# Kernel optimization log

Measured on AMD Instinct MI355X. Metric: run time of the kernel, lower is better.

The kernel has to match this reference:

```python
import jax, jax.numpy as jnp
import numpy as np

NUM_GRAPHS = 512

def setup_inputs() -> dict:
    key = jax.random.key(0)
    ks = jax.random.split(key, 16)
    N, E, F_IN, D = 50000, 800000, 128, 64
    x = jax.random.normal(ks[0], (N, F_IN), dtype=jnp.float32)
    edge_index = jax.random.randint(ks[1], (2, E), 0, N, dtype=jnp.int32)
    batch_index = jnp.sort(jax.random.randint(ks[2], (N,), 0, NUM_GRAPHS, dtype=jnp.int32))
    def lin(k, fin, fout):
        s = 1.0 / np.sqrt(fin)
        return jax.random.uniform(k, (fin, fout), jnp.float32, -s, s)
    return {
        "x": x, "edge_index": edge_index, "batch_index": batch_index,
        "W0": lin(ks[3], F_IN, D), "b0": jnp.zeros((D,), jnp.float32),
        "W1": lin(ks[4], D, D), "b1": jnp.zeros((D,), jnp.float32),
        "W2": lin(ks[5], D, D), "b2": jnp.zeros((D,), jnp.float32),
        "W3": lin(ks[6], D, D), "b3": jnp.zeros((D,), jnp.float32),
        "Wout": lin(ks[7], 2 * D, 1), "bout": jnp.zeros((1,), jnp.float32),
    }

def _gcn_edges(edge_index, N):
    # add self-loops and compute symmetric normalization D^-1/2 (A+I) D^-1/2
    loops = jnp.arange(N, dtype=edge_index.dtype)
    row = jnp.concatenate([edge_index[0], loops])  # source
    col = jnp.concatenate([edge_index[1], loops])  # target
    deg = jax.ops.segment_sum(jnp.ones_like(col, dtype=jnp.float32), col, num_segments=N)
    dinv = jnp.where(deg > 0, jax.lax.rsqrt(deg), 0.0)
    norm = dinv[row] * dinv[col]  # [E+N]
    return row, col, norm

def _gcn_conv(h, row, col, norm, W, b, N):
    h = h @ W                                   # [N, D] linear transform first
    msg = h[row] * norm[:, None]                # gather + scale
    out = jax.ops.segment_sum(msg, col, num_segments=N)  # scatter-add
    return out + b

def reference(x, edge_index, batch_index, W0, b0, W1, b1, W2, b2, W3, b3, Wout, bout):
    N = x.shape[0]
    row, col, norm = _gcn_edges(edge_index, N)
    h = jnp.tanh(_gcn_conv(x, row, col, norm, W0, b0, N))
    h = jnp.tanh(_gcn_conv(h, row, col, norm, W1, b1, N))
    h = jnp.tanh(_gcn_conv(h, row, col, norm, W2, b2, N))
    h = jnp.tanh(_gcn_conv(h, row, col, norm, W3, b3, N))
    gmax = jax.ops.segment_max(h, batch_index, num_segments=NUM_GRAPHS)
    gmax = jnp.where(jnp.isfinite(gmax), gmax, 0.0)  # empty segments -> 0
    gsum = jax.ops.segment_sum(h, batch_index, num_segments=NUM_GRAPHS)
    cnt = jax.ops.segment_sum(jnp.ones((N,), jnp.float32), batch_index, num_segments=NUM_GRAPHS)
    gmean = gsum / jnp.maximum(cnt, 1.0)[:, None]
    hidden = jnp.concatenate([gmax, gmean], axis=1)   # [G, 2D]
    out = hidden @ Wout + bout                        # [G, 1]
    return out, hidden
```

## Files before the change

### kernel.cpp

```cpp
#include <hip/hip_runtime.h>
#include <math.h>

#define CAP 64
typedef unsigned short ushort_t;
typedef unsigned int uint_t;

__global__ __launch_bounds__(256) void k_scatter2(const int* __restrict__ row,
                                                  const int* __restrict__ col, int E, int N,
                                                  int* __restrict__ deg, ushort_t* __restrict__ csr) {
    const int part = blockIdx.x & 7;
    const int slot = blockIdx.x >> 3;
    const int nslots = gridDim.x >> 3;
    const int lo = (int)((long long)N * part / 8);
    const int hi = (int)((long long)N * (part + 1) / 8);
    const int nq = E >> 2;
    for (int t = slot * blockDim.x + threadIdx.x; t < nq; t += nslots * blockDim.x) {
        int4 c = ((const int4*)col)[t];
        int4 r = ((const int4*)row)[t];
        if (c.x >= lo && c.x < hi) { int d = atomicAdd(&deg[c.x], 1); if (d < CAP) csr[((size_t)c.x << 6) + d] = (ushort_t)r.x; }
        if (c.y >= lo && c.y < hi) { int d = atomicAdd(&deg[c.y], 1); if (d < CAP) csr[((size_t)c.y << 6) + d] = (ushort_t)r.y; }
        if (c.z >= lo && c.z < hi) { int d = atomicAdd(&deg[c.z], 1); if (d < CAP) csr[((size_t)c.z << 6) + d] = (ushort_t)r.z; }
        if (c.w >= lo && c.w < hi) { int d = atomicAdd(&deg[c.w], 1); if (d < CAP) csr[((size_t)c.w << 6) + d] = (ushort_t)r.w; }
    }
    if (blockIdx.x == 0) {
        for (int e = (nq << 2) + threadIdx.x; e < E; e += blockDim.x) {
            int c = col[e];
            int d = atomicAdd(&deg[c], 1);
            if (d < CAP) csr[((size_t)c << 6) + d] = (ushort_t)row[e];
        }
    }
}

template <int K>
__global__ __launch_bounds__(256) void k_gemm(const float* __restrict__ X,
                                              const float* __restrict__ W,
                                              const int* __restrict__ deg,
                                              float* __restrict__ Gb, int N) {
    __shared__ __align__(16) float Wl[32 * 64];
    __shared__ __align__(16) float Xl[64 * 36];

    const int tid = threadIdx.x;
    const int wave = tid >> 6, lane = tid & 63;
    const int d8 = lane & 7, ns = lane >> 3;
    const int n0 = wave * 16 + ns, n1 = n0 + 8;

    const int base = blockIdx.x * 64;
    if (base >= N) return;
    const int tile_n = min(64, N - base);

    float4 a0l = {0,0,0,0}, a0h = {0,0,0,0}, a1l = {0,0,0,0}, a1h = {0,0,0,0};

    for (int kh = 0; kh < K / 32; kh++) {
        __syncthreads();
        for (int i = tid; i < 512; i += 256)
            ((float4*)Wl)[i] = ((const float4*)(W + kh * 2048))[i];
        for (int idx = tid; idx < 512; idx += 256) {
            int n = idx >> 3, q = idx & 7;
            float4 v = {0,0,0,0};
            if (n < tile_n) v = ((const float4*)(X + (size_t)(base + n) * K + kh * 32))[q];
            ((float4*)(Xl + n * 36))[q] = v;
        }
        __syncthreads();

        const float4* xq0 = (const float4*)(Xl + n0 * 36);
        const float4* xq1 = (const float4*)(Xl + n1 * 36);
        const float* wcol = Wl + d8 * 8;
#pragma unroll
        for (int kq = 0; kq < 8; kq++) {
            const float4 x4a = xq0[kq];
            const float4 x4b = xq1[kq];
            const float xs0[4] = {x4a.x, x4a.y, x4a.z, x4a.w};
            const float xs1[4] = {x4b.x, x4b.y, x4b.z, x4b.w};
#pragma unroll
            for (int j = 0; j < 4; j++) {
                const int k = kq * 4 + j;
                const float4 wa = *(const float4*)(wcol + k * 64);
                const float4 wb = *(const float4*)(wcol + k * 64 + 4);
                const float xa = xs0[j];
                const float xb = xs1[j];
                a0l.x = fmaf(xa, wa.x, a0l.x); a0l.y = fmaf(xa, wa.y, a0l.y);
                a0l.z = fmaf(xa, wa.z, a0l.z); a0l.w = fmaf(xa, wa.w, a0l.w);
                a0h.x = fmaf(xa, wb.x, a0h.x); a0h.y = fmaf(xa, wb.y, a0h.y);
                a0h.z = fmaf(xa, wb.z, a0h.z); a0h.w = fmaf(xa, wb.w, a0h.w);
                a1l.x = fmaf(xb, wa.x, a1l.x); a1l.y = fmaf(xb, wa.y, a1l.y);
                a1l.z = fmaf(xb, wa.z, a1l.z); a1l.w = fmaf(xb, wa.w, a1l.w);
                a1h.x = fmaf(xb, wb.x, a1h.x); a1h.y = fmaf(xb, wb.y, a1h.y);
                a1h.z = fmaf(xb, wb.z, a1h.z); a1h.w = fmaf(xb, wb.w, a1h.w);
            }
        }
    }

    int gn0 = base + n0, gn1 = base + n1;
    if (gn0 < N) {
        float s = rsqrtf((float)(deg[gn0] + 1));
        float4* ptr = (float4*)(Gb + (size_t)gn0 * 64);
        ptr[d8 * 2]     = make_float4(a0l.x * s, a0l.y * s, a0l.z * s, a0l.w * s);
        ptr[d8 * 2 + 1] = make_float4(a0h.x * s, a0h.y * s, a0h.z * s, a0h.w * s);
    }
    if (gn1 < N) {
        float s = rsqrtf((float)(deg[gn1] + 1));
        float4* ptr = (float4*)(Gb + (size_t)gn1 * 64);
        ptr[d8 * 2]     = make_float4(a1l.x * s, a1l.y * s, a1l.z * s, a1l.w * s);
        ptr[d8 * 2 + 1] = make_float4(a1h.x * s, a1h.y * s, a1h.z * s, a1h.w * s);
    }
}

__global__ __launch_bounds__(256) void k_agg(const float* __restrict__ Gb,
                                             const int* __restrict__ deg,
                                             const ushort_t* __restrict__ csr,
                                             const float* __restrict__ bias,
                                             float* __restrict__ H, int N) {
    const int tid = threadIdx.x;
    const int wave = tid >> 6, lane = tid & 63;
    const int s = lane >> 4;
    const int q = lane & 15;
    const int n = blockIdx.x * 16 + wave * 4 + s;
    const bool alive = (n < N);

    int cnt = 0;
    if (alive) { cnt = deg[n]; if (cnt > CAP) cnt = CAP; }
    const ushort_t* rowp = csr + ((size_t)(alive ? n : 0) << 6);

    float4 acc = {0.f, 0.f, 0.f, 0.f};
    if (alive) acc = ((const float4*)(Gb + (size_t)n * 64))[q];

    int i = 0;
    for (; i + 8 <= cnt; i += 8) {
        uint2 qa = *(const uint2*)(rowp + i);
        uint2 qb = *(const uint2*)(rowp + i + 4);
        int j0 = qa.x & 0xffff, j1 = qa.x >> 16, j2 = qa.y & 0xffff, j3 = qa.y >> 16;
        int j4 = qb.x & 0xffff, j5 = qb.x >> 16, j6 = qb.y & 0xffff, j7 = qb.y >> 16;
        float4 g0 = ((const float4*)(Gb + (size_t)j0 * 64))[q];
        float4 g1 = ((const float4*)(Gb + (size_t)j1 * 64))[q];
        float4 g2 = ((const float4*)(Gb + (size_t)j2 * 64))[q];
        float4 g3 = ((const float4*)(Gb + (size_t)j3 * 64))[q];
        float4 g4 = ((const float4*)(Gb + (size_t)j4 * 64))[q];
        float4 g5 = ((const float4*)(Gb + (size_t)j5 * 64))[q];
        float4 g6 = ((const float4*)(Gb + (size_t)j6 * 64))[q];
        float4 g7 = ((const float4*)(Gb + (size_t)j7 * 64))[q];
        float4 t0 = make_float4(g0.x + g1.x, g0.y + g1.y, g0.z + g1.z, g0.w + g1.w);
        float4 t1 = make_float4(g2.x + g3.x, g2.y + g3.y, g2.z + g3.z, g2.w + g3.w);
        float4 t2 = make_float4(g4.x + g5.x, g4.y + g5.y, g4.z + g5.z, g4.w + g5.w);
        float4 t3 = make_float4(g6.x + g7.x, g6.y + g7.y, g6.z + g7.z, g6.w + g7.w);
        acc.x += (t0.x + t1.x) + (t2.x + t3.x);
        acc.y += (t0.y + t1.y) + (t2.y + t3.y);
        acc.z += (t0.z + t1.z) + (t2.z + t3.z);
        acc.w += (t0.w + t1.w) + (t2.w + t3.w);
    }
    if (i + 4 <= cnt) {
        uint2 qa = *(const uint2*)(rowp + i);
        int j0 = qa.x & 0xffff, j1 = qa.x >> 16, j2 = qa.y & 0xffff, j3 = qa.y >> 16;
        float4 g0 = ((const float4*)(Gb + (size_t)j0 * 64))[q];
        float4 g1 = ((const float4*)(Gb + (size_t)j1 * 64))[q];
        float4 g2 = ((const float4*)(Gb + (size_t)j2 * 64))[q];
        float4 g3 = ((const float4*)(Gb + (size_t)j3 * 64))[q];
        acc.x += (g0.x + g1.x) + (g2.x + g3.x);
        acc.y += (g0.y + g1.y) + (g2.y + g3.y);
        acc.z += (g0.z + g1.z) + (g2.z + g3.z);
        acc.w += (g0.w + g1.w) + (g2.w + g3.w);
        i += 4;
    }
    if (i + 2 <= cnt) {
        uint_t qq = *(const uint_t*)(rowp + i);
        int j0 = qq & 0xffff, j1 = qq >> 16;
        float4 g0 = ((const float4*)(Gb + (size_t)j0 * 64))[q];
        float4 g1 = ((const float4*)(Gb + (size_t)j1 * 64))[q];
        acc.x += g0.x + g1.x; acc.y += g0.y + g1.y;
        acc.z += g0.z + g1.z; acc.w += g0.w + g1.w;
        i += 2;
    }
    if (i < cnt) {
        int j0 = rowp[i];
        float4 g0 = ((const float4*)(Gb + (size_t)j0 * 64))[q];
        acc.x += g0.x; acc.y += g0.y; acc.z += g0.z; acc.w += g0.w;
    }

    if (alive) {
        float dinv = rsqrtf((float)(cnt + 1));
        float4 b4 = ((const float4*)bias)[q];
        float4 r;
        r.x = tanhf(fmaf(acc.x, dinv, b4.x));
        r.y = tanhf(fmaf(acc.y, dinv, b4.y));
        r.z = tanhf(fmaf(acc.z, dinv, b4.z));
        r.w = tanhf(fmaf(acc.w, dinv, b4.w));
        ((float4*)(H + (size_t)n * 64))[q] = r;
    }
}

__global__ __launch_bounds__(256) void k_pool(const float* __restrict__ H,
                                              const int* __restrict__ batch, int N, int Gn,
                                              const float* __restrict__ Wout,
                                              const float* __restrict__ bout,
                                              float* __restrict__ out,
                                              float* __restrict__ hidden) {
    int g = blockIdx.x * 4 + (threadIdx.x >> 6);
    if (g >= Gn) return;
    int lane = threadIdx.x & 63;
    int lo = 0, hi = N;
    while (lo < hi) { int m = (lo + hi) >> 1; if (batch[m] < g) lo = m + 1; else hi = m; }
    int s = lo;
    lo = s; hi = N;
    while (lo < hi) { int m = (lo + hi) >> 1; if (batch[m] < g + 1) lo = m + 1; else hi = m; }
    int c = lo - s;

    float m0 = -INFINITY, m1 = -INFINITY, m2 = -INFINITY, m3 = -INFINITY;
    float s0 = 0.f, s1 = 0.f, s2 = 0.f, s3 = 0.f;
    int n = s;
    for (; n + 3 < s + c; n += 4) {
        float v0 = H[(size_t)n * 64 + lane];
        float v1 = H[(size_t)(n + 1) * 64 + lane];
        float v2 = H[(size_t)(n + 2) * 64 + lane];
        float v3 = H[(size_t)(n + 3) * 64 + lane];
        m0 = fmaxf(m0, v0); s0 += v0;
        m1 = fmaxf(m1, v1); s1 += v1;
        m2 = fmaxf(m2, v2); s2 += v2;
        m3 = fmaxf(m3, v3); s3 += v3;
    }
    for (; n < s + c; n++) {
        float v = H[(size_t)n * 64 + lane];
        m0 = fmaxf(m0, v); s0 += v;
    }
    float vmax = fmaxf(fmaxf(m0, m1), fmaxf(m2, m3));
    float vsum = (s0 + s1) + (s2 + s3);
    float gmax = (c > 0) ? vmax : 0.f;
    float gmean = (c > 0) ? vsum / (float)c : 0.f;
    hidden[(size_t)g * 128 + lane] = gmax;
    hidden[(size_t)g * 128 + 64 + lane] = gmean;
    float p = fmaf(gmax, Wout[lane], gmean * Wout[64 + lane]);
    for (int o = 32; o > 0; o >>= 1) p += __shfl_down(p, o);
    if (lane == 0) out[g] = p + bout[0];
}

extern "C" void kernel_launch(void* const* d_in, const int* in_sizes, int n_in,
                              void* d_out, int out_size, void* d_ws, size_t ws_size,
                              hipStream_t stream) {
    const float* x    = (const float*)d_in[0];
    const int*   ei   = (const int*)d_in[1];
    const int*   batch= (const int*)d_in[2];
    const float* W0 = (const float*)d_in[3];  const float* b0 = (const float*)d_in[4];
    const float* W1 = (const float*)d_in[5];  const float* b1 = (const float*)d_in[6];
    const float* W2 = (const float*)d_in[7];  const float* b2 = (const float*)d_in[8];
    const float* W3 = (const float*)d_in[9];  const float* b3 = (const float*)d_in[10];
    const float* Wout = (const float*)d_in[11]; const float* bout = (const float*)d_in[12];

    const int N  = in_sizes[2];
    const int E  = in_sizes[1] / 2;
    const int Gn = out_size / 129;

    const int* row = ei;
    const int* col = ei + E;

    float* out_p    = (float*)d_out;
    float* hidden_p = out_p + Gn;

    char* wp = (char*)d_ws;
    auto alloc = [&](size_t bytes) { void* p = (void*)wp; wp += (bytes + 255) & ~(size_t)255; return p; };
    int*      deg = (int*)alloc((size_t)N * 4);
    ushort_t* csr = (ushort_t*)alloc((size_t)N * CAP * 2);
    float*    Gb  = (float*)alloc((size_t)N * 64 * 4);
    float*    Hb  = (float*)alloc((size_t)N * 64 * 4);

    hipMemsetAsync(deg, 0, (size_t)N * 4, stream);
    k_scatter2<<<2048, 256, 0, stream>>>(row, col, E, N, deg, csr);

    const int gblocks = (N + 63) / 64;
    const int ablocks = (N + 15) / 16;

    k_gemm<128><<<gblocks, 256, 0, stream>>>(x, W0, deg, Gb, N);
    k_agg<<<ablocks, 256, 0, stream>>>(Gb, deg, csr, b0, Hb, N);
    k_gemm<64><<<gblocks, 256, 0, stream>>>(Hb, W1, deg, Gb, N);
    k_agg<<<ablocks, 256, 0, stream>>>(Gb, deg, csr, b1, Hb, N);
    k_gemm<64><<<gblocks, 256, 0, stream>>>(Hb, W2, deg, Gb, N);
    k_agg<<<ablocks, 256, 0, stream>>>(Gb, deg, csr, b2, Hb, N);
    k_gemm<64><<<gblocks, 256, 0, stream>>>(Hb, W3, deg, Gb, N);
    k_agg<<<ablocks, 256, 0, stream>>>(Gb, deg, csr, b3, Hb, N);

    k_pool<<<(Gn + 3) / 4, 256, 0, stream>>>(Hb, batch, N, Gn, Wout, bout, out_p, hidden_p);
}
```

Measured before the change: 327.3 us.

## Retile GEMM to 128 rows per block with 8 row accumulators per thread

The feature-transform GEMM now processes 128 nodes per block instead of 64. Each thread owns 4 output columns for 8 rows, so each weight float4 loaded from LDS is reused across 8 rows, and the output stores are coalesced float4 writes of contiguous columns. The goal is less LDS traffic per FMA and fewer blocks for the same work. In exchange the X tile in shared memory doubles and the kernel needs more accumulator registers.

```diff
diff --git a/kernel.cpp b/kernel.cpp
--- a/kernel.cpp
+++ b/kernel.cpp
@@ -37,71 +37,66 @@
                                               const int* __restrict__ deg,
                                               float* __restrict__ Gb, int N) {
     __shared__ __align__(16) float Wl[32 * 64];
-    __shared__ __align__(16) float Xl[64 * 36];
+    __shared__ __align__(16) float Xl[128 * 36];
 
     const int tid = threadIdx.x;
     const int wave = tid >> 6, lane = tid & 63;
-    const int d8 = lane & 7, ns = lane >> 3;
-    const int n0 = wave * 16 + ns, n1 = n0 + 8;
-
-    const int base = blockIdx.x * 64;
+    const int q = lane & 15;
+    const int s = lane >> 4;
+
+    const int base = blockIdx.x * 128;
     if (base >= N) return;
-    const int tile_n = min(64, N - base);
-
-    float4 a0l = {0,0,0,0}, a0h = {0,0,0,0}, a1l = {0,0,0,0}, a1h = {0,0,0,0};
+    const int tile_n = min(128, N - base);
+
+    float4 acc[8];
+#pragma unroll
+    for (int m = 0; m < 8; m++) acc[m] = make_float4(0.f, 0.f, 0.f, 0.f);
+
+    const int wbase = wave * 32;
 
     for (int kh = 0; kh < K / 32; kh++) {
         __syncthreads();
         for (int i = tid; i < 512; i += 256)
             ((float4*)Wl)[i] = ((const float4*)(W + kh * 2048))[i];
-        for (int idx = tid; idx < 512; idx += 256) {
-            int n = idx >> 3, q = idx & 7;
-            float4 v = {0,0,0,0};
-            if (n < tile_n) v = ((const float4*)(X + (size_t)(base + n) * K + kh * 32))[q];
-            ((float4*)(Xl + n * 36))[q] = v;
+        for (int idx = tid; idx < 1024; idx += 256) {
+            int n = idx >> 3, kq = idx & 7;
+            float4 v = {0.f, 0.f, 0.f, 0.f};
+            if (n < tile_n) v = ((const float4*)(X + (size_t)(base + n) * K + kh * 32))[kq];
+            ((float4*)(Xl + n * 36))[kq] = v;
         }
         __syncthreads();
 
-        const float4* xq0 = (const float4*)(Xl + n0 * 36);
-        const float4* xq1 = (const float4*)(Xl + n1 * 36);
-        const float* wcol = Wl + d8 * 8;
+        const float* wq = Wl + 4 * q;
 #pragma unroll
         for (int kq = 0; kq < 8; kq++) {
-            const float4 x4a = xq0[kq];
-            const float4 x4b = xq1[kq];
-            const float xs0[4] = {x4a.x, x4a.y, x4a.z, x4a.w};
-            const float xs1[4] = {x4b.x, x4b.y, x4b.z, x4b.w};
-#pragma unroll
-            for (int j = 0; j < 4; j++) {
-                const int k = kq * 4 + j;
-                const float4 wa = *(const float4*)(wcol + k * 64);
-                const float4 wb = *(const float4*)(wcol + k * 64 + 4);
-                const float xa = xs0[j];
-                const float xb = xs1[j];
-                a0l.x = fmaf(xa, wa.x, a0l.x); a0l.y = fmaf(xa, wa.y, a0l.y);
-                a0l.z = fmaf(xa, wa.z, a0l.z); a0l.w = fmaf(xa, wa.w, a0l.w);
-                a0h.x = fmaf(xa, wb.x, a0h.x); a0h.y = fmaf(xa, wb.y, a0h.y);
-                a0h.z = fmaf(xa, wb.z, a0h.z); a0h.w = fmaf(xa, wb.w, a0h.w);
-                a1l.x = fmaf(xb, wa.x, a1l.x); a1l.y = fmaf(xb, wa.y, a1l.y);
-                a1l.z = fmaf(xb, wa.z, a1l.z); a1l.w = fmaf(xb, wa.w, a1l.w);
-                a1h.x = fmaf(xb, wb.x, a1h.x); a1h.y = fmaf(xb, wb.y, a1h.y);
-                a1h.z = fmaf(xb, wb.z, a1h.z); a1h.w = fmaf(xb, wb.w, a1h.w);
+            const float4 w0 = *(const float4*)(wq + (kq * 4 + 0) * 64);
+            const float4 w1 = *(const float4*)(wq + (kq * 4 + 1) * 64);
+            const float4 w2 = *(const float4*)(wq + (kq * 4 + 2) * 64);
+            const float4 w3 = *(const float4*)(wq + (kq * 4 + 3) * 64);
+#pragma unroll
+            for (int m = 0; m < 8; m++) {
+                const int ln = wbase + s + 4 * m;
+                const float4 x4 = ((const float4*)(Xl + ln * 36))[kq];
+                acc[m].x = fmaf(x4.x, w0.x, acc[m].x); acc[m].y = fmaf(x4.x, w0.y, acc[m].y);
+                acc[m].z = fmaf(x4.x, w0.z, acc[m].z); acc[m].w = fmaf(x4.x, w0.w, acc[m].w);
+                acc[m].x = fmaf(x4.y, w1.x, acc[m].x); acc[m].y = fmaf(x4.y, w1.y, acc[m].y);
+                acc[m].z = fmaf(x4.y, w1.z, acc[m].z); acc[m].w = fmaf(x4.y, w1.w, acc[m].w);
+                acc[m].x = fmaf(x4.z, w2.x, acc[m].x); acc[m].y = fmaf(x4.z, w2.y, acc[m].y);
+                acc[m].z = fmaf(x4.z, w2.z, acc[m].z); acc[m].w = fmaf(x4.z, w2.w, acc[m].w);
+                acc[m].x = fmaf(x4.w, w3.x, acc[m].x); acc[m].y = fmaf(x4.w, w3.y, acc[m].y);
+                acc[m].z = fmaf(x4.w, w3.z, acc[m].z); acc[m].w = fmaf(x4.w, w3.w, acc[m].w);
             }
         }
     }
 
-    int gn0 = base + n0, gn1 = base + n1;
-    if (gn0 < N) {
-        float s = rsqrtf((float)(deg[gn0] + 1));
-        float4* ptr = (float4*)(Gb + (size_t)gn0 * 64);
-        ptr[d8 * 2]     = make_float4(a0l.x * s, a0l.y * s, a0l.z * s, a0l.w * s);
-        ptr[d8 * 2 + 1] = make_float4(a0h.x * s, a0h.y * s, a0h.z * s, a0h.w * s);
-    }
-    if (gn1 < N) {
-        float s = rsqrtf((float)(deg[gn1] + 1));
-        float4* ptr = (float4*)(Gb + (size_t)gn1 * 64);
-        ptr[d8 * 2]     = make_float4(a1l.x * s, a1l.y * s, a1l.z * s, a1l.w * s);
-        ptr[d8 * 2 + 1] = make_float4(a1h.x * s, a1h.y * s, a1h.z * s, a1h.w * s);
+#pragma unroll
+    for (int m = 0; m < 8; m++) {
+        const int gn = base + wbase + s + 4 * m;
+        if (gn < N) {
+            float sc = rsqrtf((float)(deg[gn] + 1));
+            ((float4*)(Gb + (size_t)gn * 64))[q] =
+                make_float4(acc[m].x * sc, acc[m].y * sc, acc[m].z * sc, acc[m].w * sc);
+        }
     }
 }
 
@@ -263,7 +258,7 @@
     hipMemsetAsync(deg, 0, (size_t)N * 4, stream);
     k_scatter2<<<2048, 256, 0, stream>>>(row, col, E, N, deg, csr);
 
-    const int gblocks = (N + 63) / 64;
+    const int gblocks = (N + 127) / 128;
     const int ablocks = (N + 15) / 16;
 
     k_gemm<128><<<gblocks, 256, 0, stream>>>(x, W0, deg, Gb, N);
```

After: 338.8 us. 1.03x slower.

## Fuse final aggregation with graph pooling via atomic sum and max

Applied to the files above, without the earlier changes.

The last GCN aggregation kernel now pools directly. It atomically adds each node's tanh output into per-graph sums and atomically maxes an order-preserving integer key into per-graph maxima, so the final H write and the k_pool re-read of H go away. k_pool becomes a small head kernel that reads the per-graph accumulators. The cost is heavy atomic contention, since about 100 nodes per graph hit the same 64 addresses. Float atomic summation also makes the result order-nondeterministic.

```diff
diff --git a/kernel.cpp b/kernel.cpp
--- a/kernel.cpp
+++ b/kernel.cpp
@@ -4,6 +4,14 @@
 #define CAP 64
 typedef unsigned short ushort_t;
 typedef unsigned int uint_t;
+
+__device__ __forceinline__ uint_t fkey(float f) {
+    uint_t b = __float_as_uint(f);
+    return (b & 0x80000000u) ? ~b : (b | 0x80000000u);
+}
+__device__ __forceinline__ float funkey(uint_t k) {
+    return (k & 0x80000000u) ? __uint_as_float(k ^ 0x80000000u) : __uint_as_float(~k);
+}
 
 __global__ __launch_bounds__(256) void k_scatter2(const int* __restrict__ row,
                                                   const int* __restrict__ col, int E, int N,
@@ -105,25 +113,10 @@
     }
 }
 
-__global__ __launch_bounds__(256) void k_agg(const float* __restrict__ Gb,
-                                             const int* __restrict__ deg,
-                                             const ushort_t* __restrict__ csr,
-                                             const float* __restrict__ bias,
-                                             float* __restrict__ H, int N) {
-    const int tid = threadIdx.x;
-    const int wave = tid >> 6, lane = tid & 63;
-    const int s = lane >> 4;
-    const int q = lane & 15;
-    const int n = blockIdx.x * 16 + wave * 4 + s;
-    const bool alive = (n < N);
-
-    int cnt = 0;
-    if (alive) { cnt = deg[n]; if (cnt > CAP) cnt = CAP; }
-    const ushort_t* rowp = csr + ((size_t)(alive ? n : 0) << 6);
-
-    float4 acc = {0.f, 0.f, 0.f, 0.f};
-    if (alive) acc = ((const float4*)(Gb + (size_t)n * 64))[q];
-
+__device__ __forceinline__ float4 gather4(const float* __restrict__ Gb,
+                                          const ushort_t* __restrict__ rowp,
+                                          int cnt, int n, int q) {
+    float4 acc = ((const float4*)(Gb + (size_t)n * 64))[q];
     int i = 0;
     for (; i + 8 <= cnt; i += 8) {
         uint2 qa = *(const uint2*)(rowp + i);
@@ -138,14 +131,10 @@
         float4 g5 = ((const float4*)(Gb + (size_t)j5 * 64))[q];
         float4 g6 = ((const float4*)(Gb + (size_t)j6 * 64))[q];
         float4 g7 = ((const float4*)(Gb + (size_t)j7 * 64))[q];
-        float4 t0 = make_float4(g0.x + g1.x, g0.y + g1.y, g0.z + g1.z, g0.w + g1.w);
-        float4 t1 = make_float4(g2.x + g3.x, g2.y + g3.y, g2.z + g3.z, g2.w + g3.w);
-        float4 t2 = make_float4(g4.x + g5.x, g4.y + g5.y, g4.z + g5.z, g4.w + g5.w);
-        float4 t3 = make_float4(g6.x + g7.x, g6.y + g7.y, g6.z + g7.z, g6.w + g7.w);
-        acc.x += (t0.x + t1.x) + (t2.x + t3.x);
-        acc.y += (t0.y + t1.y) + (t2.y + t3.y);
-        acc.z += (t0.z + t1.z) + (t2.z + t3.z);
-        acc.w += (t0.w + t1.w) + (t2.w + t3.w);
+        acc.x += ((g0.x + g1.x) + (g2.x + g3.x)) + ((g4.x + g5.x) + (g6.x + g7.x));
+        acc.y += ((g0.y + g1.y) + (g2.y + g3.y)) + ((g4.y + g5.y) + (g6.y + g7.y));
+        acc.z += ((g0.z + g1.z) + (g2.z + g3.z)) + ((g4.z + g5.z) + (g6.z + g7.z));
+        acc.w += ((g0.w + g1.w) + (g2.w + g3.w)) + ((g4.w + g5.w) + (g6.w + g7.w));
     }
     if (i + 4 <= cnt) {
         uint2 qa = *(const uint2*)(rowp + i);
@@ -174,20 +163,63 @@
         float4 g0 = ((const float4*)(Gb + (size_t)j0 * 64))[q];
         acc.x += g0.x; acc.y += g0.y; acc.z += g0.z; acc.w += g0.w;
     }
-
-    if (alive) {
-        float dinv = rsqrtf((float)(cnt + 1));
-        float4 b4 = ((const float4*)bias)[q];
-        float4 r;
-        r.x = tanhf(fmaf(acc.x, dinv, b4.x));
-        r.y = tanhf(fmaf(acc.y, dinv, b4.y));
-        r.z = tanhf(fmaf(acc.z, dinv, b4.z));
-        r.w = tanhf(fmaf(acc.w, dinv, b4.w));
-        ((float4*)(H + (size_t)n * 64))[q] = r;
-    }
-}
-
-__global__ __launch_bounds__(256) void k_pool(const float* __restrict__ H,
+    return acc;
+}
+
+__global__ __launch_bounds__(256) void k_agg(const float* __restrict__ Gb,
+                                             const int* __restrict__ deg,
+                                             const ushort_t* __restrict__ csr,
+                                             const float* __restrict__ bias,
+                                             float* __restrict__ H, int N) {
+    const int tid = threadIdx.x;
+    const int wave = tid >> 6, lane = tid & 63;
+    const int s = lane >> 4, q = lane & 15;
+    const int n = blockIdx.x * 16 + wave * 4 + s;
+    if (n >= N) return;
+    int cnt = deg[n]; if (cnt > CAP) cnt = CAP;
+    float4 acc = gather4(Gb, csr + ((size_t)n << 6), cnt, n, q);
+    float dinv = rsqrtf((float)(cnt + 1));
+    float4 b4 = ((const float4*)bias)[q];
+    float4 r;
+    r.x = tanhf(fmaf(acc.x, dinv, b4.x));
+    r.y = tanhf(fmaf(acc.y, dinv, b4.y));
+    r.z = tanhf(fmaf(acc.z, dinv, b4.z));
+    r.w = tanhf(fmaf(acc.w, dinv, b4.w));
+    ((float4*)(H + (size_t)n * 64))[q] = r;
+}
+
+__global__ __launch_bounds__(256) void k_aggred(const float* __restrict__ Gb,
+                                                const int* __restrict__ deg,
+                                                const ushort_t* __restrict__ csr,
+                                                const int* __restrict__ batch,
+                                                const float* __restrict__ bias,
+                                                float* __restrict__ gsum,
+                                                uint_t* __restrict__ gmaxk, int N) {
+    const int tid = threadIdx.x;
+    const int wave = tid >> 6, lane = tid & 63;
+    const int s = lane >> 4, q = lane & 15;
+    const int n = blockIdx.x * 16 + wave * 4 + s;
+    if (n >= N) return;
+    int cnt = deg[n]; if (cnt > CAP) cnt = CAP;
+    float4 acc = gather4(Gb, csr + ((size_t)n << 6), cnt, n, q);
+    float dinv = rsqrtf((float)(cnt + 1));
+    float4 b4 = ((const float4*)bias)[q];
+    float4 r;
+    r.x = tanhf(fmaf(acc.x, dinv, b4.x));
+    r.y = tanhf(fmaf(acc.y, dinv, b4.y));
+    r.z = tanhf(fmaf(acc.z, dinv, b4.z));
+    r.w = tanhf(fmaf(acc.w, dinv, b4.w));
+    const int g = batch[n];
+    float* sp = gsum + (size_t)g * 64 + 4 * q;
+    atomicAdd(sp + 0, r.x); atomicAdd(sp + 1, r.y);
+    atomicAdd(sp + 2, r.z); atomicAdd(sp + 3, r.w);
+    uint_t* mp = gmaxk + (size_t)g * 64 + 4 * q;
+    atomicMax(mp + 0, fkey(r.x)); atomicMax(mp + 1, fkey(r.y));
+    atomicMax(mp + 2, fkey(r.z)); atomicMax(mp + 3, fkey(r.w));
+}
+
+__global__ __launch_bounds__(256) void k_head(const float* __restrict__ gsum,
+                                              const uint_t* __restrict__ gmaxk,
                                               const int* __restrict__ batch, int N, int Gn,
                                               const float* __restrict__ Wout,
                                               const float* __restrict__ bout,
@@ -203,27 +235,11 @@
     while (lo < hi) { int m = (lo + hi) >> 1; if (batch[m] < g + 1) lo = m + 1; else hi = m; }
     int c = lo - s;
 
-    float m0 = -INFINITY, m1 = -INFINITY, m2 = -INFINITY, m3 = -INFINITY;
-    float s0 = 0.f, s1 = 0.f, s2 = 0.f, s3 = 0.f;
-    int n = s;
-    for (; n + 3 < s + c; n += 4) {
-        float v0 = H[(size_t)n * 64 + lane];
-        float v1 = H[(size_t)(n + 1) * 64 + lane];
-        float v2 = H[(size_t)(n + 2) * 64 + lane];
-        float v3 = H[(size_t)(n + 3) * 64 + lane];
-        m0 = fmaxf(m0, v0); s0 += v0;
-        m1 = fmaxf(m1, v1); s1 += v1;
-        m2 = fmaxf(m2, v2); s2 += v2;
-        m3 = fmaxf(m3, v3); s3 += v3;
-    }
-    for (; n < s + c; n++) {
-        float v = H[(size_t)n * 64 + lane];
-        m0 = fmaxf(m0, v); s0 += v;
-    }
-    float vmax = fmaxf(fmaxf(m0, m1), fmaxf(m2, m3));
-    float vsum = (s0 + s1) + (s2 + s3);
-    float gmax = (c > 0) ? vmax : 0.f;
-    float gmean = (c > 0) ? vsum / (float)c : 0.f;
+    float gmax = 0.f, gmean = 0.f;
+    if (c > 0) {
+        gmax = funkey(gmaxk[(size_t)g * 64 + lane]);
+        gmean = gsum[(size_t)g * 64 + lane] / (float)c;
+    }
     hidden[(size_t)g * 128 + lane] = gmax;
     hidden[(size_t)g * 128 + 64 + lane] = gmean;
     float p = fmaf(gmax, Wout[lane], gmean * Wout[64 + lane]);
@@ -255,12 +271,15 @@
 
     char* wp = (char*)d_ws;
     auto alloc = [&](size_t bytes) { void* p = (void*)wp; wp += (bytes + 255) & ~(size_t)255; return p; };
-    int*      deg = (int*)alloc((size_t)N * 4);
-    ushort_t* csr = (ushort_t*)alloc((size_t)N * CAP * 2);
-    float*    Gb  = (float*)alloc((size_t)N * 64 * 4);
-    float*    Hb  = (float*)alloc((size_t)N * 64 * 4);
-
-    hipMemsetAsync(deg, 0, (size_t)N * 4, stream);
+    int*      deg   = (int*)alloc((size_t)N * 4);
+    float*    gsum  = (float*)alloc((size_t)Gn * 64 * 4);
+    uint_t*   gmaxk = (uint_t*)alloc((size_t)Gn * 64 * 4);
+    ushort_t* csr   = (ushort_t*)alloc((size_t)N * CAP * 2);
+    float*    Gb    = (float*)alloc((size_t)N * 64 * 4);
+    float*    Hb    = (float*)alloc((size_t)N * 64 * 4);
+
+    size_t zbytes = (size_t)((char*)(gmaxk + (size_t)Gn * 64) - (char*)deg);
+    hipMemsetAsync(deg, 0, zbytes, stream);
     k_scatter2<<<2048, 256, 0, stream>>>(row, col, E, N, deg, csr);
 
     const int gblocks = (N + 63) / 64;
@@ -273,7 +292,7 @@
     k_gemm<64><<<gblocks, 256, 0, stream>>>(Hb, W2, deg, Gb, N);
     k_agg<<<ablocks, 256, 0, stream>>>(Gb, deg, csr, b2, Hb, N);
     k_gemm<64><<<gblocks, 256, 0, stream>>>(Hb, W3, deg, Gb, N);
-    k_agg<<<ablocks, 256, 0, stream>>>(Gb, deg, csr, b3, Hb, N);
-
-    k_pool<<<(Gn + 3) / 4, 256, 0, stream>>>(Hb, batch, N, Gn, Wout, bout, out_p, hidden_p);
-}
+    k_aggred<<<ablocks, 256, 0, stream>>>(Gb, deg, csr, batch, b3, gsum, gmaxk, N);
+
+    k_head<<<(Gn + 3) / 4, 256, 0, stream>>>(gsum, gmaxk, batch, N, Gn, Wout, bout, out_p, hidden_p);
+}
```

Result: slower. 410.6 us (+25.4%).
